# Kernel optimization log

Hardware: AMD Instinct MI355X
Metric: run time of the kernel (lower is better)

## Reference

```python
import jax, jax.numpy as jnp
from jax import lax
import numpy as np

B, C, T = 16, 512, 4096
COEFF_INIT = 0.04


def setup_inputs() -> dict:
    key = jax.random.key(0)
    k1, k2 = jax.random.split(key)
    x = jax.random.normal(k1, (B, C, T), dtype=jnp.float32)
    # learned per-channel smoothing coefficients, initialized like the module
    weights = jnp.ones((C,), dtype=jnp.float32) * COEFF_INIT
    return {"x": x, "weights": weights}


def reference(x, weights):
    # clamp weights to [0, 1] (mirrors the in-place no-grad clamp; values stay
    # unchanged here since coeff_init is inside the range)
    s = jnp.clip(weights, 0.0, 1.0)  # [C]
    xt = jnp.moveaxis(x, 2, 0)       # [T, B, C]
    init = xt[0]                      # y_0 = x_0

    def step(acc, sample):
        acc = s * sample + (1.0 - s) * acc
        return acc, acc

    _, ys = lax.scan(step, init, xt[1:])          # [T-1, B, C]
    out = jnp.concatenate([init[None], ys], axis=0)  # [T, B, C]
    return jnp.moveaxis(out, 0, 2)                   # [B, C, T]
```

## Files before the change

kernel.cpp:

```cpp
#include <hip/hip_runtime.h>


constexpr int T_LEN = 4096;
constexpr int C_LEN = 512;
constexpr int BLOCK = 1024;
constexpr int NWAVES = BLOCK / 64;

__global__ __launch_bounds__(BLOCK) void ema_scan_kernel(
    const float* __restrict__ x,
    const float* __restrict__ w,
    float* __restrict__ y)
{
    const int row  = blockIdx.x;
    const int c    = row & (C_LEN - 1);
    const int tid  = threadIdx.x;
    const int lane = tid & 63;
    const int wave = tid >> 6;

    float s = w[c];
    s = fminf(fmaxf(s, 0.0f), 1.0f);
    const float a = 1.0f - s;

    const float4* xr = (const float4*)(x + (size_t)row * T_LEN) + tid;
    float4*       yr = (float4*)(y + (size_t)row * T_LEN) + tid;

    float4 v = *xr;

    float l0 = (tid == 0) ? v.x : s * v.x;
    float l1 = fmaf(a, l0, s * v.y);
    float l2 = fmaf(a, l1, s * v.z);
    float l3 = fmaf(a, l2, s * v.w);

    const float a2 = a * a;
    const float a3 = a2 * a;
    const float a4 = a2 * a2;

    float S = l3;
    float wgt = a4;
    #pragma unroll
    for (int d = 1; d < 64; d <<= 1) {
        float up = __shfl_up(S, d, 64);
        if (lane >= d) S = fmaf(wgt, up, S);
        wgt *= wgt;
    }
    const float a256 = wgt;

    __shared__ float tot[NWAVES];
    if (lane == 63) tot[wave] = S;
    __syncthreads();

    float Cw = 0.0f;
    {
        float f = 1.0f;
        for (int u = wave - 1; u >= 0; --u) {
            Cw = fmaf(f, tot[u], Cw);
            f *= a256;
        }
    }

    float Sx = __shfl_up(S, 1, 64);
    float Pl = (lane == 0) ? 0.0f : Sx;
    float powl = 1.0f, tq = a4;
    #pragma unroll
    for (int b = 0; b < 6; ++b) {
        if ((lane >> b) & 1) powl *= tq;
        tq *= tq;
    }
    const float P = fmaf(powl, Cw, Pl);

    float4 o;
    o.x = fmaf(a,  P, l0);
    o.y = fmaf(a2, P, l1);
    o.z = fmaf(a3, P, l2);
    o.w = fmaf(a4, P, l3);
    *yr = o;
}

extern "C" void kernel_launch(void* const* d_in, const int* in_sizes, int n_in,
                              void* d_out, int out_size, void* d_ws, size_t ws_size,
                              hipStream_t stream) {
    const float* x = (const float*)d_in[0];
    const float* w = (const float*)d_in[1];
    float* y = (float*)d_out;

    const int rows = out_size / T_LEN;
    ema_scan_kernel<<<rows, BLOCK, 0, stream>>>(x, y != nullptr ? w : w, y);
}
```

Measured before the change: 224.1 us.

## Process each row with one wave over 16 chunks, removing block-wide sync

Each row is now handled by a single 64-lane wave that loads 16 float4 chunks per lane, scans each chunk with wave shuffles, and carries the prefix between chunks serially in registers. Four rows share a 256-thread block. This removes the shared-memory exchange and __syncthreads of the old 1024-thread-per-row design, along with its serial cross-wave combine. In exchange each lane holds many more registers (16 float4 plus 16 partial sums), which may reduce occupancy, and the shuffle count per lane grows.

```diff
diff --git a/kernel.cpp b/kernel.cpp
--- a/kernel.cpp
+++ b/kernel.cpp
@@ -3,77 +3,81 @@
 
 constexpr int T_LEN = 4096;
 constexpr int C_LEN = 512;
-constexpr int BLOCK = 1024;
-constexpr int NWAVES = BLOCK / 64;
+constexpr int WAVES_PER_BLOCK = 4;
+constexpr int BLOCK = 64 * WAVES_PER_BLOCK;
+constexpr int CHUNKS = 16;
 
-__global__ __launch_bounds__(BLOCK) void ema_scan_kernel(
+__global__ __launch_bounds__(BLOCK, 4) void ema_wave_kernel(
     const float* __restrict__ x,
     const float* __restrict__ w,
     float* __restrict__ y)
 {
-    const int row  = blockIdx.x;
+    const int wave = threadIdx.x >> 6;
+    const int lane = threadIdx.x & 63;
+    const int row  = blockIdx.x * WAVES_PER_BLOCK + wave;
     const int c    = row & (C_LEN - 1);
-    const int tid  = threadIdx.x;
-    const int lane = tid & 63;
-    const int wave = tid >> 6;
 
     float s = w[c];
     s = fminf(fmaxf(s, 0.0f), 1.0f);
     const float a = 1.0f - s;
 
-    const float4* xr = (const float4*)(x + (size_t)row * T_LEN) + tid;
-    float4*       yr = (float4*)(y + (size_t)row * T_LEN) + tid;
+    const float4* xp = (const float4*)(x + (size_t)row * T_LEN);
+    float4*       yp = (float4*)(y + (size_t)row * T_LEN);
 
-    float4 v = *xr;
+    float4 v[CHUNKS];
+    #pragma unroll
+    for (int k = 0; k < CHUNKS; ++k)
+        v[k] = xp[(k << 6) + lane];
 
-    float l0 = (tid == 0) ? v.x : s * v.x;
-    float l1 = fmaf(a, l0, s * v.y);
-    float l2 = fmaf(a, l1, s * v.z);
-    float l3 = fmaf(a, l2, s * v.w);
+    const float a2 = a * a, a3 = a2 * a, a4 = a2 * a2;
 
-    const float a2 = a * a;
-    const float a3 = a2 * a;
-    const float a4 = a2 * a2;
+    float S[CHUNKS];
+    #pragma unroll
+    for (int k = 0; k < CHUNKS; ++k) {
+        float l0 = s * v[k].x;
+        if (k == 0 && lane == 0) l0 = v[0].x;
+        float l1 = fmaf(a, l0, s * v[k].y);
+        float l2 = fmaf(a, l1, s * v[k].z);
+        float l3 = fmaf(a, l2, s * v[k].w);
+        v[k].x = l0; v[k].y = l1; v[k].z = l2; v[k].w = l3;
+        S[k] = l3;
+    }
 
-    float S = l3;
     float wgt = a4;
     #pragma unroll
     for (int d = 1; d < 64; d <<= 1) {
-        float up = __shfl_up(S, d, 64);
-        if (lane >= d) S = fmaf(wgt, up, S);
+        #pragma unroll
+        for (int k = 0; k < CHUNKS; ++k) {
+            float up = __shfl_up(S[k], d, 64);
+            if (lane >= d) S[k] = fmaf(wgt, up, S[k]);
+        }
         wgt *= wgt;
     }
     const float a256 = wgt;
 
-    __shared__ float tot[NWAVES];
-    if (lane == 63) tot[wave] = S;
-    __syncthreads();
-
-    float Cw = 0.0f;
-    {
-        float f = 1.0f;
-        for (int u = wave - 1; u >= 0; --u) {
-            Cw = fmaf(f, tot[u], Cw);
-            f *= a256;
-        }
-    }
-
-    float Sx = __shfl_up(S, 1, 64);
-    float Pl = (lane == 0) ? 0.0f : Sx;
     float powl = 1.0f, tq = a4;
     #pragma unroll
     for (int b = 0; b < 6; ++b) {
         if ((lane >> b) & 1) powl *= tq;
         tq *= tq;
     }
-    const float P = fmaf(powl, Cw, Pl);
 
-    float4 o;
-    o.x = fmaf(a,  P, l0);
-    o.y = fmaf(a2, P, l1);
-    o.z = fmaf(a3, P, l2);
-    o.w = fmaf(a4, P, l3);
-    *yr = o;
+    float Ek = 0.0f;
+    #pragma unroll
+    for (int k = 0; k < CHUNKS; ++k) {
+        float Sx = __shfl_up(S[k], 1, 64);
+        float base = (lane == 0) ? 0.0f : Sx;
+        float P = fmaf(powl, Ek, base);
+        float4 o;
+        o.x = fmaf(a,  P, v[k].x);
+        o.y = fmaf(a2, P, v[k].y);
+        o.z = fmaf(a3, P, v[k].z);
+        o.w = fmaf(a4, P, v[k].w);
+        yp[(k << 6) + lane] = o;
+
+        float Tk = __shfl(S[k], 63, 64);
+        Ek = fmaf(a256, Ek, Tk);
+    }
 }
 
 extern "C" void kernel_launch(void* const* d_in, const int* in_sizes, int n_in,
@@ -84,5 +88,6 @@
     float* y = (float*)d_out;
 
     const int rows = out_size / T_LEN;
-    ema_scan_kernel<<<rows, BLOCK, 0, stream>>>(x, y != nullptr ? w : w, y);
+    const int grid = rows / WAVES_PER_BLOCK;
+    ema_wave_kernel<<<grid, BLOCK, 0, stream>>>(x, w, y);
 }
```

Measured after the change: 235.4 us. +5.0%, slower.
